# Kernel optimization log

Hardware: AMD Instinct MI355X
Metric: run time of the kernel (lower is better)

## Reference

```python
import jax, jax.numpy as jnp
import numpy as np

B, N, C = 8, 16384, 4
NUM_GROUPS = 512   # K for farthest point sampling
GROUP_SIZE = 32    # K after energy-based top-k
UPSCALE_K = 512    # ball-query candidate count
RADIUS = 0.5       # group_radius
CONTEXT = 256      # context_length


def _fps_idx(xyz, lengths, K):
    """Iterative farthest point sampling. xyz: (B,P,3). Returns (B,K) int32 indices.
    Start point is index 0 (random_start_point=False). Assumes lengths >= K."""
    Bn, P, _ = xyz.shape
    valid = jnp.arange(P)[None, :] < lengths[:, None]
    start = jnp.zeros((Bn,), jnp.int32)
    mind0 = jnp.full((Bn, P), jnp.float32(1e10))

    def step(carry, _):
        mind, last = carry
        lastpt = jnp.take_along_axis(xyz, last[:, None, None], axis=1)  # (B,1,3)
        d = jnp.sum((xyz - lastpt) ** 2, axis=-1)                       # (B,P)
        mind = jnp.minimum(mind, d)
        nxt = jnp.argmax(jnp.where(valid, mind, -jnp.inf), axis=1).astype(jnp.int32)
        return (mind, nxt), nxt

    _, rest = jax.lax.scan(step, (mind0, start), None, length=K - 1)  # (K-1,B)
    return jnp.concatenate([start[:, None], rest.T], axis=1)          # (B,K)


def _masked_gather(points, idx):
    """torch masked_gather: -1 indices are replaced with 0 before gathering."""
    idx0 = jnp.maximum(idx, 0)
    if idx.ndim == 3:
        Bn, G, K = idx.shape
        out = jnp.take_along_axis(points, idx0.reshape(Bn, G * K)[:, :, None], axis=1)
        return out.reshape(Bn, G, K, points.shape[-1])
    return jnp.take_along_axis(points, idx0[:, :, None], axis=1)


def _ball_query(centers, xyz, lengths, K, radius):
    """First-K points within radius of each center, in original index order; pad -1."""
    P = xyz.shape[1]
    d2 = jnp.sum((centers[:, :, None, :] - xyz[:, None, :, :]) ** 2, axis=-1)  # (B,G,P)
    valid = (d2 < radius * radius) & (jnp.arange(P)[None, None, :] < lengths[:, None, None])
    # key = -index for valid points, -P for invalid -> top_k gives first valid indices
    key = jnp.where(valid, -jnp.arange(P, dtype=jnp.int32)[None, None, :], jnp.int32(-P))
    vals, pos = jax.lax.top_k(key, K)           # (B,G,K)
    return jnp.where(vals > -P, pos, -1)


def _topk_by_energy(points, idx, K):
    """Keep the K highest-energy (channel 3) points per group; pad -1."""
    Bn, G, Ko = idx.shape
    e = points[..., 3]                                                  # (B,P)
    eb = jnp.broadcast_to(e[:, None, :], (Bn, G, e.shape[1]))
    energies = jnp.take_along_axis(eb, jnp.maximum(idx, 0), axis=2)     # (B,G,Ko)
    energies = jnp.where(idx == -1, -jnp.inf, energies)
    top_e, top_pos = jax.lax.top_k(energies, K)
    top_idx = jnp.take_along_axis(idx, top_pos, axis=2)
    return jnp.where(jnp.isneginf(top_e), -1, top_idx)


def setup_inputs() -> dict:
    key = jax.random.key(0)
    k1, k2 = jax.random.split(key)
    points = jax.random.normal(k1, (B, N, C), dtype=jnp.float32)
    lengths = jax.random.randint(k2, (B,), 3 * N // 4, N + 1, dtype=jnp.int32)
    return {"points": points, "lengths": lengths}


def reference(points, lengths):
    # FPS -> group centers (kept with all C channels, as in masked_gather(points, idx))
    centers_idx = _fps_idx(points[:, :, :3], lengths, NUM_GROUPS)
    group_centers = _masked_gather(points, centers_idx)                 # (B,G,C)
    # Ball query around centers
    idx = _ball_query(group_centers[:, :, :3], points[:, :, :3], lengths, UPSCALE_K, RADIUS)
    # Energy-based reduction to GROUP_SIZE points per group
    idx = _topk_by_energy(points, idx, GROUP_SIZE)                      # (B,G,Ks)
    point_lengths = jnp.sum(idx != -1, axis=2)                          # (B,G)
    # fill_empty_indices: replace -1 with the group's first index
    filled = jnp.where(idx == -1, idx[:, :, :1], idx)
    groups = _masked_gather(points, filled)                             # (B,G,Ks,C)
    point_mask = jnp.arange(GROUP_SIZE)[None, None, :] < point_lengths[:, :CONTEXT, None]
    G = idx.shape[1]
    group_lengths = jnp.sum(jnp.all(idx != -1, axis=2), axis=1)         # (B,)
    embedding_mask = jnp.arange(G)[None, :] < group_lengths[:, None]
    return (groups[:, :CONTEXT], group_centers[:, :CONTEXT],
            embedding_mask[:, :CONTEXT], point_mask)
```

## Files before the change

kernel.cpp:

```cpp
#include <hip/hip_runtime.h>
#include <stdint.h>

#define NB   8
#define NP   16384
#define NG   512
#define GS   32
#define UPK  512
#define CTX  256

#define OFF_CENTERS (NB*CTX*GS*4)
#define OFF_EMB     (OFF_CENTERS + NB*CTX*4)
#define OFF_PMASK   (OFF_EMB + NB*CTX)

typedef unsigned long long u64;
typedef unsigned int u32;

__device__ __forceinline__ u32 fkey(float f) {
  union { float f; u32 u; } v; v.f = f;
  u32 s = v.u;
  return s ^ ((s & 0x80000000u) ? 0xFFFFFFFFu : 0x80000000u);
}

__device__ __forceinline__ float dist2(float ax, float ay, float az,
                                       float bx, float by, float bz) {
  float dx = __fsub_rn(ax, bx);
  float dy = __fsub_rn(ay, by);
  float dz = __fsub_rn(az, bz);
  return __fadd_rn(__fadd_rn(__fmul_rn(dx, dx), __fmul_rn(dy, dy)),
                   __fmul_rn(dz, dz));
}

template<int CTRL, int RM>
__device__ __forceinline__ u64 dpp_max_u64(u64 k) {
  int lo = (int)(u32)k, hi = (int)(u32)(k >> 32);
  int mlo = __builtin_amdgcn_update_dpp(lo, lo, CTRL, RM, 0xf, false);
  int mhi = __builtin_amdgcn_update_dpp(hi, hi, CTRL, RM, 0xf, false);
  u64 o = ((u64)(u32)mhi << 32) | (u32)mlo;
  return o > k ? o : k;
}

__device__ __forceinline__ u64 wave_max_u64(u64 k) {
  k = dpp_max_u64<0x111, 0xf>(k);
  k = dpp_max_u64<0x112, 0xf>(k);
  k = dpp_max_u64<0x114, 0xf>(k);
  k = dpp_max_u64<0x118, 0xf>(k);
  k = dpp_max_u64<0x142, 0xa>(k);
  k = dpp_max_u64<0x143, 0xc>(k);
  return k;
}

__device__ __forceinline__ u64 read_lane_u64(u64 k, int lane) {
  u32 lo = (u32)__builtin_amdgcn_readlane((int)(u32)k, lane);
  u32 hi = (u32)__builtin_amdgcn_readlane((int)(u32)(k >> 32), lane);
  return ((u64)hi << 32) | lo;
}

#define FPS_T 512
#define PPT   (NP / FPS_T)

__global__ __launch_bounds__(FPS_T)
__attribute__((amdgpu_waves_per_eu(2, 2)))
void fps_kernel(const float4* __restrict__ pts, const int* __restrict__ lengths,
                float4* __restrict__ centers_ws, int* __restrict__ group_len,
                float* __restrict__ out)
{
  const int b    = blockIdx.x;
  const int tid  = threadIdx.x;
  const int lane = tid & 63;
  const int wave = tid >> 6;
  const float4* p = pts + (size_t)b * NP;
  const int len = lengths[b];
  if (tid == 0) group_len[b] = 0;

  const float4 q0 = p[0];
  float px[PPT], py[PPT], pz[PPT], mind[PPT];
#pragma unroll
  for (int j = 0; j < PPT; j++) {
    int i = tid + j * FPS_T;
    float4 q = p[i];
    if (i >= len) q = q0;
    px[j] = q.x; py[j] = q.y; pz[j] = q.z;
    mind[j] = 1e10f;
  }

  __shared__ u64 sred[2][8];
  __shared__ int s_centers[NG];
  if (tid == 0) s_centers[0] = 0;

  int last = 0;
  for (int it = 1; it < NG; it++) {
    float4 lp = p[last];
    float tmax = -1.0f; int tj = 0;
#pragma unroll
    for (int j = 0; j < PPT; j++) {
      float d = dist2(px[j], py[j], pz[j], lp.x, lp.y, lp.z);
      float m = fminf(mind[j], d);
      mind[j] = m;
      bool c = m > tmax;
      tmax = c ? m : tmax;
      tj   = c ? j : tj;
    }
    int gidx = tid + (tj << 9);
    u64 key = ((u64)__float_as_uint(tmax) << 32) | (u32)(~gidx);
    key = wave_max_u64(key);
    u64 wkey = read_lane_u64(key, 63);
    if (lane == 0) sred[it & 1][wave] = wkey;
    __syncthreads();
    u64 k2 = sred[it & 1][lane & 7];
    k2 = dpp_max_u64<0x111, 0xf>(k2);
    k2 = dpp_max_u64<0x112, 0xf>(k2);
    k2 = dpp_max_u64<0x114, 0xf>(k2);
    u64 bk = read_lane_u64(k2, 7);
    last = (int)(~(u32)bk) & (NP - 1);
    if (tid == 0) s_centers[it] = last;
  }
  __syncthreads();

  {
    int ci = s_centers[tid] & (NP - 1);
    float4 q = p[ci];
    centers_ws[b * NG + tid] = q;
    if (tid < CTX) {
      ((float4*)(out + OFF_CENTERS))[b * CTX + tid] = q;
    }
  }
}

#define BQ_T 256

__global__ __launch_bounds__(BQ_T)
void group_kernel(const float4* __restrict__ pts, const int* __restrict__ lengths,
                  const float4* __restrict__ centers_ws, int* __restrict__ group_len,
                  float* __restrict__ out)
{
  const int blk  = blockIdx.x;
  const int b    = blk & (NB - 1);
  const int g    = blk >> 3;
  const int tid  = threadIdx.x;
  const int lane = tid & 63;
  const int wave = tid >> 6;
  const float4* p = pts + (size_t)b * NP;
  const int len = lengths[b];
  const float4 cc = centers_ws[b * NG + g];

  __shared__ u64 masks[256];
  __shared__ u32 scnt[256];
  __shared__ u32 spre[256];
  __shared__ u32 swsum[4];
  __shared__ float candE[UPK];
  __shared__ int   candI[UPK];
  __shared__ int   s_T, s_pl;
  __shared__ int   s_win[GS];

  if (g >= CTX) {
    u32 c = 0;
    for (int step = 0; step < 64; step++) {
      int i = step * 256 + tid;
      if (i < len) {
        float4 q = p[i];
        float d = dist2(cc.x, cc.y, cc.z, q.x, q.y, q.z);
        c += (d < 0.25f) ? 1u : 0u;
      }
    }
#pragma unroll
    for (int off = 32; off; off >>= 1) c += __shfl_down(c, (unsigned)off, 64);
    if (lane == 0) swsum[wave] = c;
    __syncthreads();
    if (tid == 0) {
      u32 total = swsum[0] + swsum[1] + swsum[2] + swsum[3];
      if (total >= GS) atomicAdd(&group_len[b], 1);
    }
    return;
  }

  for (int step = 0; step < 64; step++) {
    int i = step * 256 + tid;
    bool flag = false;
    if (i < len) {
      float4 q = p[i];
      float d = dist2(cc.x, cc.y, cc.z, q.x, q.y, q.z);
      flag = d < 0.25f;
    }
    u64 m = __ballot(flag);
    if (lane == 0) masks[step * 4 + wave] = m;
  }
  __syncthreads();

  u32 cnt = (u32)__popcll(masks[tid]);
  u32 s = cnt;
#pragma unroll
  for (int off = 1; off < 64; off <<= 1) {
    u32 o = __shfl_up(s, (unsigned)off, 64);
    if (lane >= off) s += o;
  }
  if (lane == 63) swsum[wave] = s;
  __syncthreads();
  u32 woff = 0;
#pragma unroll
  for (int w = 0; w < 4; w++) woff += (w < wave) ? swsum[w] : 0u;
  const u32 total = swsum[0] + swsum[1] + swsum[2] + swsum[3];
  const u32 incl = s + woff;
  scnt[tid] = cnt;
  spre[tid] = incl;

  if (total > UPK) {
    u32 ex = incl - cnt;
    if (ex <= (UPK - 1) && incl > (UPK - 1)) {
      u32 r = (UPK - 1) - ex;
      u64 m = masks[tid];
      for (u32 k = 0; k < r; k++) m &= m - 1;
      s_T = tid * 64 + ((int)__ffsll((unsigned long long)m) - 1);
    }
  } else if (tid == 0) {
    s_T = NP - 1;
  }
  __syncthreads();
  const int T = s_T;

  for (int step = 0; step < 64; step++) {
    int i  = step * 256 + tid;
    int ch = step * 4 + wave;
    u64 m = masks[ch];
    if (((m >> lane) & 1ull) && i <= T) {
      u32 pos = ((spre[ch] - scnt[ch]) +
                 (u32)__popcll(m & ((1ull << lane) - 1ull))) & (UPK - 1);
      candE[pos] = ((const float*)p)[i * 4 + 3];
      candI[pos] = i;
    }
  }
  __syncthreads();

  const int ncand = (int)(total < UPK ? total : UPK);

  if (wave == 0) {
    u64 k[8];
#pragma unroll
    for (int t = 0; t < 8; t++) {
      int ci = lane + t * 64;
      k[t] = (ci < ncand) ? (((u64)fkey(candE[ci]) << 32) | (u32)(~ci)) : 0ull;
    }
    int pl = 0;
    for (int r = 0; r < GS; r++) {
      u64 bm = k[0];
#pragma unroll
      for (int t = 1; t < 8; t++) if (k[t] > bm) bm = k[t];
#pragma unroll
      for (int off = 32; off; off >>= 1) {
        u64 o = __shfl_xor(bm, (unsigned)off, 64);
        if (o > bm) bm = o;
      }
      if (bm == 0) break;
      int pos = (int)(~(u32)bm) & (UPK - 1);
      if (lane == 0) s_win[r] = candI[pos];
      int ol = pos & 63, ot = pos >> 6;
#pragma unroll
      for (int t = 0; t < 8; t++)
        if (t == ot && lane == ol) k[t] = 0;
      pl = r + 1;
    }
    if (lane == 0) {
      int f0 = (pl > 0) ? s_win[0] : 0;
      for (int r = pl; r < GS; r++) s_win[r] = f0;
      s_pl = pl;
    }
  }
  __syncthreads();

  const int base = b * CTX + g;
  if (tid < GS) {
    int fi = s_win[tid] & (NP - 1);
    float4 q = p[fi];
    ((float4*)out)[base * GS + tid] = q;
    out[OFF_PMASK + base * GS + tid] = (tid < s_pl) ? 1.0f : 0.0f;
  }
  if (tid == 0 && total >= GS) atomicAdd(&group_len[b], 1);
}

__global__ void emb_kernel(const int* __restrict__ group_len,
                           float* __restrict__ out)
{
  int i = blockIdx.x * blockDim.x + threadIdx.x;
  if (i < NB * CTX) {
    int b = i >> 8;
    int g = i & 255;
    out[OFF_EMB + i] = (g < group_len[b]) ? 1.0f : 0.0f;
  }
}

extern "C" void kernel_launch(void* const* d_in, const int* in_sizes, int n_in,
                              void* d_out, int out_size, void* d_ws, size_t ws_size,
                              hipStream_t stream)
{
  const float4* pts     = (const float4*)d_in[0];
  const int*    lengths = (const int*)d_in[1];
  float* out = (float*)d_out;

  float4* centers_ws = (float4*)d_ws;
  int*    group_len  = (int*)((char*)d_ws + (size_t)NB * NG * sizeof(float4));

  fps_kernel<<<NB, FPS_T, 0, stream>>>(pts, lengths, centers_ws, group_len, out);
  group_kernel<<<NB * NG, BQ_T, 0, stream>>>(pts, lengths, centers_ws, group_len, out);
  emb_kernel<<<(NB * CTX + 255) / 256, 256, 0, stream>>>(group_len, out);
}
```

Baseline: 733.8 us.

## Split FPS per batch across four blocks with global atomic argmax exchange

The farthest-point-sampling loop for each batch now runs on four workgroups instead of one, each holding a quarter of the points in registers. Every iteration each block publishes its best key with a global atomicMax, then spins on a per-iteration counter until all four blocks have arrived before reading the winning index. A memset clears the slots and counters on each launch. The aim is to use more CUs for the serial FPS phase, at the price of a global-memory barrier on every one of the 511 iterations. It also depends on all 32 blocks being co-resident, otherwise the spin can deadlock or only exit through its guard.

```diff
diff --git a/kernel.cpp b/kernel.cpp
--- a/kernel.cpp
+++ b/kernel.cpp
@@ -11,6 +11,13 @@
 #define OFF_CENTERS (NB*CTX*GS*4)
 #define OFF_EMB     (OFF_CENTERS + NB*CTX*4)
 #define OFF_PMASK   (OFF_EMB + NB*CTX)
+
+#define WS_CENTERS   0
+#define WS_GLEN      65536
+#define WS_SLOT      65600
+#define WS_CNT       98368
+#define WS_ZERO_FROM 65536
+#define WS_ZERO_LEN  (114752 - 65536)
 
 typedef unsigned long long u64;
 typedef unsigned int u32;
@@ -55,28 +62,37 @@
   return ((u64)hi << 32) | lo;
 }
 
+#define FB    4
 #define FPS_T 512
-#define PPT   (NP / FPS_T)
+#define PPT   (NP / (FPS_T * FB))
+#define STRIDE NP_OVER_FB
+#define NP_OVER_FB (NP / FB)
 
 __global__ __launch_bounds__(FPS_T)
-__attribute__((amdgpu_waves_per_eu(2, 2)))
 void fps_kernel(const float4* __restrict__ pts, const int* __restrict__ lengths,
                 float4* __restrict__ centers_ws, int* __restrict__ group_len,
+                u64* __restrict__ slots, u32* __restrict__ cnts,
                 float* __restrict__ out)
 {
-  const int b    = blockIdx.x;
+  const int blk  = blockIdx.x;
+  const int b    = blk & (NB - 1);
+  const int sub  = blk >> 3;
   const int tid  = threadIdx.x;
   const int lane = tid & 63;
   const int wave = tid >> 6;
+  const int base = sub * NP_OVER_FB;
   const float4* p = pts + (size_t)b * NP;
   const int len = lengths[b];
-  if (tid == 0) group_len[b] = 0;
+  if (sub == 0 && tid == 0) group_len[b] = 0;
+
+  u64* __restrict__ slot = slots + b * NG;
+  u32* __restrict__ cnt  = cnts  + b * NG;
 
   const float4 q0 = p[0];
   float px[PPT], py[PPT], pz[PPT], mind[PPT];
 #pragma unroll
   for (int j = 0; j < PPT; j++) {
-    int i = tid + j * FPS_T;
+    int i = base + tid + j * FPS_T;
     float4 q = p[i];
     if (i >= len) q = q0;
     px[j] = q.x; py[j] = q.y; pz[j] = q.z;
@@ -84,6 +100,7 @@
   }
 
   __shared__ u64 sred[2][8];
+  __shared__ int s_last;
   __shared__ int s_centers[NG];
   if (tid == 0) s_centers[0] = 0;
 
@@ -100,7 +117,7 @@
       tmax = c ? m : tmax;
       tj   = c ? j : tj;
     }
-    int gidx = tid + (tj << 9);
+    int gidx = base + tid + (tj << 9);
     u64 key = ((u64)__float_as_uint(tmax) << 32) | (u32)(~gidx);
     key = wave_max_u64(key);
     u64 wkey = read_lane_u64(key, 63);
@@ -111,12 +128,25 @@
     k2 = dpp_max_u64<0x112, 0xf>(k2);
     k2 = dpp_max_u64<0x114, 0xf>(k2);
     u64 bk = read_lane_u64(k2, 7);
-    last = (int)(~(u32)bk) & (NP - 1);
+
+    if (tid == 0) {
+      atomicMax(&slot[it], bk);
+      __threadfence();
+      atomicAdd(&cnt[it], 1u);
+      int guard = 0;
+      while (atomicAdd(&cnt[it], 0u) < FB && ++guard < (1 << 26)) {
+        __builtin_amdgcn_s_sleep(2);
+      }
+      u64 g = atomicAdd(&slot[it], 0ull);
+      s_last = (int)(~(u32)g) & (NP - 1);
+    }
+    __syncthreads();
+    last = s_last;
     if (tid == 0) s_centers[it] = last;
   }
   __syncthreads();
 
-  {
+  if (sub == 0) {
     int ci = s_centers[tid] & (NP - 1);
     float4 q = p[ci];
     centers_ws[b * NG + tid] = q;
@@ -295,10 +325,17 @@
   const int*    lengths = (const int*)d_in[1];
   float* out = (float*)d_out;
 
-  float4* centers_ws = (float4*)d_ws;
-  int*    group_len  = (int*)((char*)d_ws + (size_t)NB * NG * sizeof(float4));
-
-  fps_kernel<<<NB, FPS_T, 0, stream>>>(pts, lengths, centers_ws, group_len, out);
-  group_kernel<<<NB * NG, BQ_T, 0, stream>>>(pts, lengths, centers_ws, group_len, out);
+  char* ws = (char*)d_ws;
+  float4* centers_ws = (float4*)(ws + WS_CENTERS);
+  int*    group_len  = (int*)(ws + WS_GLEN);
+  u64*    slots      = (u64*)(ws + WS_SLOT);
+  u32*    cnts       = (u32*)(ws + WS_CNT);
+
+  hipMemsetAsync(ws + WS_ZERO_FROM, 0, WS_ZERO_LEN, stream);
+
+  fps_kernel<<<NB * FB, FPS_T, 0, stream>>>(pts, lengths, centers_ws,
+                                            group_len, slots, cnts, out);
+  group_kernel<<<NB * NG, BQ_T, 0, stream>>>(pts, lengths, centers_ws,
+                                             group_len, out);
   emb_kernel<<<(NB * CTX + 255) / 256, 256, 0, stream>>>(group_len, out);
 }
```

Measured after the change: 1.071 ms. +46.0%, slower.
